# Kernel tuning notes

Hardware: AMD Instinct MI355X
Metric: run time of the kernel (lower is better)

## Reference

```python
import jax, jax.numpy as jnp
import numpy as np

B, S, D = 4, 2048, 1024

def setup_inputs() -> dict:
    key = jax.random.key(0)
    ks = jax.random.split(key, 7)
    scale = 1.0 / np.sqrt(D)
    return {
        "x": jax.random.normal(ks[0], (B, S, D), dtype=jnp.float32),
        "Wq": jax.random.uniform(ks[1], (D, D), jnp.float32, -scale, scale),
        "bq": jax.random.uniform(ks[2], (D,), jnp.float32, -scale, scale),
        "Wk": jax.random.uniform(ks[3], (D, D), jnp.float32, -scale, scale),
        "bk": jax.random.uniform(ks[4], (D,), jnp.float32, -scale, scale),
        "Wv": jax.random.uniform(ks[5], (D, D), jnp.float32, -scale, scale),
        "bv": jax.random.uniform(ks[6], (D,), jnp.float32, -scale, scale),
    }

def reference(x, Wq, bq, Wk, bk, Wv, bv):
    # Linear layers: x @ W^T + b (torch nn.Linear convention)
    q = jnp.einsum('bsd,ed->bse', x, Wq) + bq  # [B,S,D]
    k = jnp.einsum('bsd,ed->bse', x, Wk) + bk
    v = jnp.einsum('bsd,ed->bse', x, Wv) + bv
    inv_sqrt_d = 1.0 / jnp.sqrt(jnp.asarray(k.shape[-1], k.dtype))
    scores = jnp.einsum('bqd,bkd->bqk', q, k) * inv_sqrt_d  # [B,S,S]
    attn = jax.nn.softmax(scores, axis=-1)
    return jnp.einsum('bqk,bkd->bqd', attn, v)
```

## Files before the change

kernel.cpp:

```cpp
#include <hip/hip_runtime.h>
#include <cstdint>


typedef __bf16 bf16x8_t __attribute__((ext_vector_type(8)));
typedef float  f32x4_t  __attribute__((ext_vector_type(4)));
typedef int    i32x8_t  __attribute__((ext_vector_type(8)));
typedef int    i32x4_t  __attribute__((ext_vector_type(4)));

__device__ __forceinline__ uint16_t f2bf(float f) {
    union { float f; uint32_t u; } v; v.f = f;
    return (uint16_t)((v.u + 0x7fffu + ((v.u >> 16) & 1u)) >> 16);
}

__device__ __forceinline__ uint8_t f2fp8(float f) {
    union { float f; uint32_t u; } v; v.f = f;
    const uint32_t sgn = (v.u >> 31) << 7;
    const uint32_t mag = v.u & 0x7fffffffu;
    uint32_t out;
    if (mag < 0x3c800000u) {
        out = (uint32_t)__builtin_rintf(__builtin_fabsf(f) * 512.0f);
    } else {
        uint32_t t = mag + 0x7ffffu + ((mag >> 20) & 1u);
        out = (t >> 20) - 960u;
        if (out > 0x7eu) out = 0x7eu;
    }
    return (uint8_t)(sgn | out);
}

__device__ __forceinline__ void gload_lds16(const void* g, void* lds) {
    __builtin_amdgcn_global_load_lds(
        (const __attribute__((address_space(1))) void*)g,
        (__attribute__((address_space(3))) void*)lds, 16, 0, 0);
}

template <int EPI, typename OutT>
__global__ __launch_bounds__(256, 4) void gemm_bt(
    const uint16_t* __restrict__ A, int lda, long long sAz,
    const uint16_t* __restrict__ B, int ldb, long long sBz,
    OutT* __restrict__ C, int ldc, long long sCz,
    const float* __restrict__ bias0, const float* __restrict__ bias1,
    float* __restrict__ gsum, int K, float alpha)
{
    __shared__ uint16_t ldsA[128 * 64];
    __shared__ uint16_t ldsB[128 * 64];
    __shared__ float inv_denom[128];

    const int tid  = threadIdx.x;
    const int wave = tid >> 6;
    const int lane = tid & 63;
    const int quad = lane >> 4;
    const int l15  = lane & 15;
    const int z    = blockIdx.z;

    A += (long long)z * sAz;
    B += (long long)z * sBz;
    C += (long long)z * sCz;

    const int m0 = blockIdx.x * 128;
    const int n0 = blockIdx.y * 128;

    if (EPI == 4) {
        if (tid < 128) {
            const float* gp = gsum + (long long)z * 32768 + (m0 + tid) * 16;
            float s = 0.f;
#pragma unroll
            for (int t = 0; t < 16; ++t) s += gp[t];
            inv_denom[tid] = 1.f / s;
        }
    }

    const uint16_t* gA[4];
    const uint16_t* gB[4];
    uint16_t* lA[4];
    uint16_t* lB[4];
#pragma unroll
    for (int c = 0; c < 4; ++c) {
        const int s   = (c * 4 + wave) * 64 + lane;
        const int r   = s >> 3;
        const int col = ((s & 7) ^ (r & 7)) * 8;
        gA[c] = A + (long long)(m0 + r) * lda + col;
        gB[c] = B + (long long)(n0 + r) * ldb + col;
        lA[c] = ldsA + (c * 4 + wave) * 512;
        lB[c] = ldsB + (c * 4 + wave) * 512;
    }

    const int m_off = (wave & 1) * 64;
    const int n_off = (wave >> 1) * 64;

    f32x4_t acc[4][4];
#pragma unroll
    for (int i = 0; i < 4; ++i)
#pragma unroll
        for (int j = 0; j < 4; ++j)
            acc[i][j] = f32x4_t{0.f, 0.f, 0.f, 0.f};

    for (int k0 = 0; k0 < K; k0 += 64) {
#pragma unroll
        for (int c = 0; c < 4; ++c) gload_lds16(gA[c], lA[c]);
#pragma unroll
        for (int c = 0; c < 4; ++c) gload_lds16(gB[c], lB[c]);
#pragma unroll
        for (int c = 0; c < 4; ++c) { gA[c] += 64; gB[c] += 64; }
        __syncthreads();

#pragma unroll
        for (int t = 0; t < 2; ++t) {
            const int csw = ((t * 4 + quad) ^ (l15 & 7)) * 8;
            bf16x8_t af[4], bfr[4];
#pragma unroll
            for (int i = 0; i < 4; ++i)
                af[i] = *(const bf16x8_t*)(ldsA + (m_off + i * 16 + l15) * 64 + csw);
#pragma unroll
            for (int j = 0; j < 4; ++j)
                bfr[j] = *(const bf16x8_t*)(ldsB + (n_off + j * 16 + l15) * 64 + csw);
#pragma unroll
            for (int i = 0; i < 4; ++i)
#pragma unroll
                for (int j = 0; j < 4; ++j)
                    acc[i][j] = __builtin_amdgcn_mfma_f32_16x16x32_bf16(af[i], bfr[j], acc[i][j], 0, 0, 0);
        }
        __syncthreads();
    }

    if (EPI == 1 || EPI == 2) {
        const float* bias = (z == 0) ? bias0 : bias1;
#pragma unroll
        for (int i = 0; i < 4; ++i) {
            const int mb = m0 + m_off + i * 16 + quad * 4;
            float rb[4];
            if (EPI == 2) {
#pragma unroll
                for (int r = 0; r < 4; ++r) rb[r] = bias[mb + r];
            }
#pragma unroll
            for (int j = 0; j < 4; ++j) {
                const int n = n0 + n_off + j * 16 + l15;
                const float cb = (EPI == 1) ? bias[n] : 0.f;
#pragma unroll
                for (int r = 0; r < 4; ++r) {
                    const float v = acc[i][j][r] + ((EPI == 1) ? cb : rb[r]);
                    if (sizeof(OutT) == 1)
                        ((uint8_t*)C)[(long long)(mb + r) * ldc + n] = f2fp8(v);
                    else
                        ((uint16_t*)C)[(long long)(mb + r) * ldc + n] = f2bf(v);
                }
            }
        }
    } else {
#pragma unroll
        for (int i = 0; i < 4; ++i) {
            const int rl = m_off + i * 16 + quad * 4;
            const int mb = m0 + rl;
#pragma unroll
            for (int j = 0; j < 4; ++j) {
                const int n = n0 + n_off + j * 16 + l15;
#pragma unroll
                for (int r = 0; r < 4; ++r)
                    ((float*)C)[(long long)(mb + r) * ldc + n] =
                        acc[i][j][r] * inv_denom[rl + r];
            }
        }
    }
}

__global__ __launch_bounds__(256, 3) void score_f8(
    const uint8_t* __restrict__ Qf8, const uint8_t* __restrict__ Kf8,
    uint16_t* __restrict__ P, float* __restrict__ gsum, float alpha)
{
    __shared__ uint8_t ldsA[128 * 128];
    __shared__ uint8_t ldsB[128 * 128];

    const int tid  = threadIdx.x;
    const int wave = tid >> 6;
    const int lane = tid & 63;
    const int quad = lane >> 4;
    const int l15  = lane & 15;
    const int z    = blockIdx.z;

    const uint8_t* A = Qf8 + (long long)z * 2097152;
    const uint8_t* B = Kf8 + (long long)z * 2097152;
    uint16_t* C = P + (long long)z * 4194304;

    const int m0 = blockIdx.x * 128;
    const int n0 = blockIdx.y * 128;

    const uint8_t* gA[4];
    const uint8_t* gB[4];
    uint8_t* lA[4];
    uint8_t* lB[4];
#pragma unroll
    for (int c = 0; c < 4; ++c) {
        const int s   = (c * 4 + wave) * 64 + lane;
        const int r   = s >> 3;
        const int col = ((s & 7) ^ (r & 7)) * 16;
        gA[c] = A + (long long)(m0 + r) * 1024 + col;
        gB[c] = B + (long long)(n0 + r) * 1024 + col;
        lA[c] = ldsA + (c * 4 + wave) * 1024;
        lB[c] = ldsB + (c * 4 + wave) * 1024;
    }

    const int m_off = (wave & 1) * 64;
    const int n_off = (wave >> 1) * 64;

    f32x4_t acc[4][4];
#pragma unroll
    for (int i = 0; i < 4; ++i)
#pragma unroll
        for (int j = 0; j < 4; ++j)
            acc[i][j] = f32x4_t{0.f, 0.f, 0.f, 0.f};

    const int h0 = quad * 2;
    const int h1 = quad * 2 + 1;

    for (int k0 = 0; k0 < 1024; k0 += 128) {
#pragma unroll
        for (int c = 0; c < 4; ++c) gload_lds16(gA[c], lA[c]);
#pragma unroll
        for (int c = 0; c < 4; ++c) gload_lds16(gB[c], lB[c]);
#pragma unroll
        for (int c = 0; c < 4; ++c) { gA[c] += 128; gB[c] += 128; }
        __syncthreads();

        i32x8_t af[4], bfr[4];
#pragma unroll
        for (int i = 0; i < 4; ++i) {
            const int m = m_off + i * 16 + l15;
            const int sw = m & 7;
            const i32x4_t lo = *(const i32x4_t*)(ldsA + m * 128 + (h0 ^ sw) * 16);
            const i32x4_t hi = *(const i32x4_t*)(ldsA + m * 128 + (h1 ^ sw) * 16);
            af[i] = i32x8_t{lo[0], lo[1], lo[2], lo[3], hi[0], hi[1], hi[2], hi[3]};
        }
#pragma unroll
        for (int j = 0; j < 4; ++j) {
            const int n = n_off + j * 16 + l15;
            const int sw = n & 7;
            const i32x4_t lo = *(const i32x4_t*)(ldsB + n * 128 + (h0 ^ sw) * 16);
            const i32x4_t hi = *(const i32x4_t*)(ldsB + n * 128 + (h1 ^ sw) * 16);
            bfr[j] = i32x8_t{lo[0], lo[1], lo[2], lo[3], hi[0], hi[1], hi[2], hi[3]};
        }
#pragma unroll
        for (int i = 0; i < 4; ++i)
#pragma unroll
            for (int j = 0; j < 4; ++j)
                acc[i][j] = __builtin_amdgcn_mfma_scale_f32_16x16x128_f8f6f4(
                    af[i], bfr[j], acc[i][j],
                    0, 0,
                    0, 0x7f7f7f7f,
                    0, 0x7f7f7f7f);
        __syncthreads();
    }

    float rs[4][4];
#pragma unroll
    for (int i = 0; i < 4; ++i)
#pragma unroll
        for (int r = 0; r < 4; ++r) rs[i][r] = 0.f;
#pragma unroll
    for (int i = 0; i < 4; ++i) {
        const int mb = m0 + m_off + i * 16 + quad * 4;
#pragma unroll
        for (int j = 0; j < 4; ++j) {
            const int n = n0 + n_off + j * 16 + l15;
#pragma unroll
            for (int r = 0; r < 4; ++r) {
                const float e = exp2f(acc[i][j][r] * alpha);
                rs[i][r] += e;
                C[(long long)(mb + r) * 2048 + n] = f2bf(e);
            }
        }
    }
#pragma unroll
    for (int m = 1; m < 16; m <<= 1)
#pragma unroll
        for (int i = 0; i < 4; ++i)
#pragma unroll
            for (int r = 0; r < 4; ++r)
                rs[i][r] += __shfl_xor(rs[i][r], m);
    float* lp = (float*)ldsA;
    if (l15 == 0) {
#pragma unroll
        for (int i = 0; i < 4; ++i)
#pragma unroll
            for (int r = 0; r < 4; ++r)
                lp[wave * 64 + i * 16 + quad * 4 + r] = rs[i][r];
    }
    __syncthreads();
    if (tid < 128) {
        const float s = lp[(tid >> 6) * 64 + (tid & 63)] +
                        lp[((tid >> 6) + 2) * 64 + (tid & 63)];
        gsum[(long long)z * 32768 + (m0 + tid) * 16 + blockIdx.y] = s;
    }
}

__global__ void cvt_all(const float* __restrict__ x,
                        const float* __restrict__ Wq, const float* __restrict__ Wk,
                        const float* __restrict__ Wv,
                        uint16_t* __restrict__ x_bf, uint16_t* __restrict__ w_bf) {
    const int b = blockIdx.x;
    const float* src;
    uint16_t* dst;
    int i;
    if (b < 8192) {
        src = x; dst = x_bf; i = b * 256 + threadIdx.x;
    } else {
        const int wz = (b - 8192) >> 10;
        const int rb = (b - 8192) & 1023;
        src = (wz == 0) ? Wq : (wz == 1) ? Wk : Wv;
        dst = w_bf + (long long)wz * 1048576;
        i = rb * 256 + threadIdx.x;
    }
    const float4 f = ((const float4*)src)[i];
    ushort4 o;
    o.x = f2bf(f.x); o.y = f2bf(f.y); o.z = f2bf(f.z); o.w = f2bf(f.w);
    ((ushort4*)dst)[i] = o;
}

extern "C" void kernel_launch(void* const* d_in, const int* in_sizes, int n_in,
                              void* d_out, int out_size, void* d_ws, size_t ws_size,
                              hipStream_t stream) {
    const float* x  = (const float*)d_in[0];
    const float* Wq = (const float*)d_in[1];
    const float* bq = (const float*)d_in[2];
    const float* Wk = (const float*)d_in[3];
    const float* bk = (const float*)d_in[4];
    const float* Wv = (const float*)d_in[5];
    const float* bv = (const float*)d_in[6];
    float* out = (float*)d_out;

    char* w = (char*)d_ws;
    uint16_t* x_bf = (uint16_t*)(w);
    float*    gsum = (float*)(w);
    uint16_t* w_bf = (uint16_t*)(w + 16777216);
    uint8_t*  Qf8  = (uint8_t*)(w + 23068672);
    uint8_t*  Kf8  = (uint8_t*)(w + 31457280);
    uint16_t* Vt   = (uint16_t*)(w + 39845888);
    uint16_t* Pb   = (uint16_t*)(w + 56623104);

    cvt_all<<<11264, 256, 0, stream>>>(x, Wq, Wk, Wv, x_bf, w_bf);

    gemm_bt<1, uint8_t><<<dim3(64, 8, 2), 256, 0, stream>>>(
        x_bf, 1024, 0LL,
        w_bf, 1024, 1048576LL,
        Qf8, 1024, 8388608LL,
        bq, bk, nullptr, 1024, 1.0f);

    gemm_bt<2, uint16_t><<<dim3(8, 64, 1), 256, 0, stream>>>(
        w_bf + 2097152, 1024, 0LL,
        x_bf, 1024, 0LL,
        Vt, 8192, 0LL,
        bv, bv, nullptr, 1024, 1.0f);

    score_f8<<<dim3(16, 16, 4), 256, 0, stream>>>(
        Qf8, Kf8, Pb, gsum, 0.045084222f);

    gemm_bt<4, float><<<dim3(16, 8, 4), 256, 0, stream>>>(
        Pb, 2048, 4194304LL,
        Vt, 8192, 2048LL,
        out, 1024, 2097152LL,
        nullptr, nullptr, gsum, 2048, 1.0f);
}
```

Before: 235.6 us.

## Replace bf16 GEMM with 512-thread double-buffered pipelined kernel using 256-row tiles

The 128x128 single-buffered GEMM used for the Q/K, V and PV products is replaced by an 8-wave kernel with 256xBN tiles. LDS is double-buffered and global-to-LDS loads for upcoming k-tiles are interleaved with MFMA phases using explicit barriers, waitcnts and setprio. The aim is to hide load latency behind compute and raise data reuse per block. In exchange it uses more LDS and registers, has fewer blocks per launch (grid occupancy risk on the smaller GEMMs), and relies on hand-tuned vmcnt counts that are fragile.

New measurement: 260.6 us. 10.6% more time.

```diff
diff --git a/kernel.cpp b/kernel.cpp
--- a/kernel.cpp
+++ b/kernel.cpp
@@ -33,34 +33,44 @@
         (__attribute__((address_space(3))) void*)lds, 16, 0, 0);
 }
 
-template <int EPI, typename OutT>
-__global__ __launch_bounds__(256, 4) void gemm_bt(
+#define BAR()   asm volatile("s_barrier" ::: "memory")
+#define WLGKM() asm volatile("s_waitcnt lgkmcnt(0)" ::: "memory")
+
+template <int BN, int EPI, typename OutT>
+__global__ __launch_bounds__(512, 2) void gemm8p(
     const uint16_t* __restrict__ A, int lda, long long sAz,
     const uint16_t* __restrict__ B, int ldb, long long sBz,
     OutT* __restrict__ C, int ldc, long long sCz,
     const float* __restrict__ bias0, const float* __restrict__ bias1,
-    float* __restrict__ gsum, int K, float alpha)
+    const float* __restrict__ gsum, int K)
 {
-    __shared__ uint16_t ldsA[128 * 64];
-    __shared__ uint16_t ldsB[128 * 64];
-    __shared__ float inv_denom[128];
+    constexpr int NF    = BN / 64;
+    constexpr int LB    = BN / 128;
+    constexpr int BSLOT = BN * 128;
+    constexpr int BKH   = BN * 64;
+
+    __shared__ uint16_t ldsA[32768];
+    __shared__ uint16_t ldsB[BN * 128];
+    __shared__ float    inv_denom[256];
 
     const int tid  = threadIdx.x;
-    const int wave = tid >> 6;
+    const int wv   = tid >> 6;
     const int lane = tid & 63;
     const int quad = lane >> 4;
     const int l15  = lane & 15;
+    const int wm   = wv >> 2;
+    const int wn   = wv & 3;
     const int z    = blockIdx.z;
 
     A += (long long)z * sAz;
     B += (long long)z * sBz;
     C += (long long)z * sCz;
 
-    const int m0 = blockIdx.x * 128;
-    const int n0 = blockIdx.y * 128;
+    const int m0 = blockIdx.x * 256;
+    const int n0 = blockIdx.y * BN;
 
     if (EPI == 4) {
-        if (tid < 128) {
+        if (tid < 256) {
             const float* gp = gsum + (long long)z * 32768 + (m0 + tid) * 16;
             float s = 0.f;
 #pragma unroll
@@ -69,95 +79,158 @@
         }
     }
 
-    const uint16_t* gA[4];
-    const uint16_t* gB[4];
-    uint16_t* lA[4];
-    uint16_t* lB[4];
-#pragma unroll
-    for (int c = 0; c < 4; ++c) {
-        const int s   = (c * 4 + wave) * 64 + lane;
-        const int r   = s >> 3;
-        const int col = ((s & 7) ^ (r & 7)) * 8;
-        gA[c] = A + (long long)(m0 + r) * lda + col;
-        gB[c] = B + (long long)(n0 + r) * ldb + col;
-        lA[c] = ldsA + (c * 4 + wave) * 512;
-        lB[c] = ldsB + (c * 4 + wave) * 512;
-    }
-
-    const int m_off = (wave & 1) * 64;
-    const int n_off = (wave >> 1) * 64;
-
-    f32x4_t acc[4][4];
-#pragma unroll
-    for (int i = 0; i < 4; ++i)
-#pragma unroll
-        for (int j = 0; j < 4; ++j)
-            acc[i][j] = f32x4_t{0.f, 0.f, 0.f, 0.f};
-
-    for (int k0 = 0; k0 < K; k0 += 64) {
-#pragma unroll
-        for (int c = 0; c < 4; ++c) gload_lds16(gA[c], lA[c]);
-#pragma unroll
-        for (int c = 0; c < 4; ++c) gload_lds16(gB[c], lB[c]);
-#pragma unroll
-        for (int c = 0; c < 4; ++c) { gA[c] += 64; gB[c] += 64; }
-        __syncthreads();
-
-#pragma unroll
-        for (int t = 0; t < 2; ++t) {
-            const int csw = ((t * 4 + quad) ^ (l15 & 7)) * 8;
-            bf16x8_t af[4], bfr[4];
-#pragma unroll
-            for (int i = 0; i < 4; ++i)
-                af[i] = *(const bf16x8_t*)(ldsA + (m_off + i * 16 + l15) * 64 + csw);
-#pragma unroll
-            for (int j = 0; j < 4; ++j)
-                bfr[j] = *(const bf16x8_t*)(ldsB + (n_off + j * 16 + l15) * 64 + csw);
-#pragma unroll
-            for (int i = 0; i < 4; ++i)
-#pragma unroll
-                for (int j = 0; j < 4; ++j)
-                    acc[i][j] = __builtin_amdgcn_mfma_f32_16x16x32_bf16(af[i], bfr[j], acc[i][j], 0, 0, 0);
-        }
-        __syncthreads();
+    const int r  = tid >> 2;
+    const int ca = (tid & 3) ^ ((tid >> 4) & 3);
+    const uint16_t* aS = A + (long long)(m0 + r) * lda + ca * 8;
+    const uint16_t* bS = B + (long long)(n0 + r) * ldb + ca * 8;
+    const int dOf = wv * 1024;
+
+    auto STAGE_A = [&](int kt, int h, int sl) {
+        const uint16_t* s = aS + kt * 64 + h * 32;
+        char* d = (char*)ldsA + sl * 32768 + h * 16384 + dOf;
+        gload_lds16(s, d);
+        gload_lds16(s + (long long)128 * lda, d + 8192);
+    };
+    auto STAGE_B = [&](int kt, int h, int sl) {
+        const uint16_t* s = bS + kt * 64 + h * 32;
+        char* d = (char*)ldsB + sl * BSLOT + h * BKH + dOf;
+        gload_lds16(s, d);
+        if (LB == 2) gload_lds16(s + (long long)128 * ldb, d + 8192);
+    };
+
+    const int csw  = ((quad ^ (l15 >> 2)) & 3) * 16;
+    const int aOff = (wm * 128 + l15) * 64 + csw;
+    const int bOff = (wn * (BN / 4) + l15) * 64 + csw;
+
+    f32x4_t acc[8][NF];
+#pragma unroll
+    for (int i = 0; i < 8; ++i)
+#pragma unroll
+        for (int j = 0; j < NF; ++j) acc[i][j] = f32x4_t{0.f, 0.f, 0.f, 0.f};
+
+    const int NT = K >> 6;
+
+    STAGE_B(0, 0, 0); STAGE_A(0, 0, 0); STAGE_B(0, 1, 0); STAGE_A(0, 1, 0);
+    STAGE_B(1, 0, 1); STAGE_A(1, 0, 1); STAGE_B(1, 1, 1);
+    if constexpr (LB == 2) asm volatile("s_waitcnt vmcnt(6)" ::: "memory");
+    else                   asm volatile("s_waitcnt vmcnt(4)" ::: "memory");
+    BAR();
+
+    for (int t = 0; t < NT; ++t) {
+        const int sl = t & 1;
+        const int so = sl ^ 1;
+        const int t1 = (t + 1 < NT) ? t + 1 : 0;
+        const int t2 = (t + 2 < NT) ? t + 2 : 0;
+        const char* Ab = (const char*)ldsA + sl * 32768;
+        const char* Bb = (const char*)ldsB + sl * BSLOT;
+
+        bf16x8_t af[4], bfv[NF];
+
+#pragma unroll
+        for (int i = 0; i < 4; ++i)
+            af[i] = *(const bf16x8_t*)(Ab + i * 1024 + aOff);
+#pragma unroll
+        for (int j = 0; j < NF; ++j)
+            bfv[j] = *(const bf16x8_t*)(Bb + j * 1024 + bOff);
+        STAGE_A(t1, 1, so);
+        BAR(); WLGKM();
+        __builtin_amdgcn_s_setprio(1);
+#pragma unroll
+        for (int i = 0; i < 4; ++i)
+#pragma unroll
+            for (int j = 0; j < NF; ++j)
+                acc[i][j] = __builtin_amdgcn_mfma_f32_16x16x32_bf16(
+                    af[i], bfv[j], acc[i][j], 0, 0, 0);
+        __builtin_amdgcn_s_setprio(0);
+        BAR();
+
+#pragma unroll
+        for (int i = 0; i < 4; ++i)
+            af[i] = *(const bf16x8_t*)(Ab + 4096 + i * 1024 + aOff);
+        STAGE_B(t2, 0, sl);
+        BAR(); WLGKM();
+        __builtin_amdgcn_s_setprio(1);
+#pragma unroll
+        for (int i = 0; i < 4; ++i)
+#pragma unroll
+            for (int j = 0; j < NF; ++j)
+                acc[4 + i][j] = __builtin_amdgcn_mfma_f32_16x16x32_bf16(
+                    af[i], bfv[j], acc[4 + i][j], 0, 0, 0);
+        __builtin_amdgcn_s_setprio(0);
+        BAR();
+
+#pragma unroll
+        for (int i = 0; i < 4; ++i)
+            af[i] = *(const bf16x8_t*)(Ab + 16384 + i * 1024 + aOff);
+#pragma unroll
+        for (int j = 0; j < NF; ++j)
+            bfv[j] = *(const bf16x8_t*)(Bb + BKH + j * 1024 + bOff);
+        STAGE_A(t2, 0, sl);
+        BAR(); WLGKM();
+        __builtin_amdgcn_s_setprio(1);
+#pragma unroll
+        for (int i = 0; i < 4; ++i)
+#pragma unroll
+            for (int j = 0; j < NF; ++j)
+                acc[i][j] = __builtin_amdgcn_mfma_f32_16x16x32_bf16(
+                    af[i], bfv[j], acc[i][j], 0, 0, 0);
+        __builtin_amdgcn_s_setprio(0);
+        BAR();
+
+#pragma unroll
+        for (int i = 0; i < 4; ++i)
+            af[i] = *(const bf16x8_t*)(Ab + 16384 + 4096 + i * 1024 + aOff);
+        STAGE_B(t2, 1, sl);
+        BAR(); WLGKM();
+        __builtin_amdgcn_s_setprio(1);
+#pragma unroll
+        for (int i = 0; i < 4; ++i)
+#pragma unroll
+            for (int j = 0; j < NF; ++j)
+                acc[4 + i][j] = __builtin_amdgcn_mfma_f32_16x16x32_bf16(
+                    af[i], bfv[j], acc[4 + i][j], 0, 0, 0);
+        __builtin_amdgcn_s_setprio(0);
+        if constexpr (LB == 2) asm volatile("s_waitcnt vmcnt(6)" ::: "memory");
+        else                   asm volatile("s_waitcnt vmcnt(4)" ::: "memory");
+        BAR();
     }
 
     if (EPI == 1 || EPI == 2) {
         const float* bias = (z == 0) ? bias0 : bias1;
 #pragma unroll
-        for (int i = 0; i < 4; ++i) {
-            const int mb = m0 + m_off + i * 16 + quad * 4;
+        for (int fi = 0; fi < 8; ++fi) {
+            const int mb = m0 + wm * 128 + fi * 16 + quad * 4;
             float rb[4];
             if (EPI == 2) {
 #pragma unroll
-                for (int r = 0; r < 4; ++r) rb[r] = bias[mb + r];
+                for (int rr = 0; rr < 4; ++rr) rb[rr] = bias[mb + rr];
             }
 #pragma unroll
-            for (int j = 0; j < 4; ++j) {
-                const int n = n0 + n_off + j * 16 + l15;
+            for (int fj = 0; fj < NF; ++fj) {
+                const int n = n0 + wn * (BN / 4) + fj * 16 + l15;
                 const float cb = (EPI == 1) ? bias[n] : 0.f;
 #pragma unroll
-                for (int r = 0; r < 4; ++r) {
-                    const float v = acc[i][j][r] + ((EPI == 1) ? cb : rb[r]);
+                for (int rr = 0; rr < 4; ++rr) {
+                    const float vv = acc[fi][fj][rr] + ((EPI == 1) ? cb : rb[rr]);
                     if (sizeof(OutT) == 1)
-                        ((uint8_t*)C)[(long long)(mb + r) * ldc + n] = f2fp8(v);
+                        ((uint8_t*)C)[(long long)(mb + rr) * ldc + n] = f2fp8(vv);
                     else
-                        ((uint16_t*)C)[(long long)(mb + r) * ldc + n] = f2bf(v);
+                        ((uint16_t*)C)[(long long)(mb + rr) * ldc + n] = f2bf(vv);
                 }
             }
         }
     } else {
 #pragma unroll
-        for (int i = 0; i < 4; ++i) {
-            const int rl = m_off + i * 16 + quad * 4;
+        for (int fi = 0; fi < 8; ++fi) {
+            const int rl = wm * 128 + fi * 16 + quad * 4;
             const int mb = m0 + rl;
 #pragma unroll
-            for (int j = 0; j < 4; ++j) {
-                const int n = n0 + n_off + j * 16 + l15;
-#pragma unroll
-                for (int r = 0; r < 4; ++r)
-                    ((float*)C)[(long long)(mb + r) * ldc + n] =
-                        acc[i][j][r] * inv_denom[rl + r];
+            for (int fj = 0; fj < NF; ++fj) {
+                const int n = n0 + wn * (BN / 4) + fj * 16 + l15;
+#pragma unroll
+                for (int rr = 0; rr < 4; ++rr)
+                    ((float*)C)[(long long)(mb + rr) * ldc + n] =
+                        acc[fi][fj][rr] * inv_denom[rl + rr];
             }
         }
     }
@@ -338,24 +411,24 @@
 
     cvt_all<<<11264, 256, 0, stream>>>(x, Wq, Wk, Wv, x_bf, w_bf);
 
-    gemm_bt<1, uint8_t><<<dim3(64, 8, 2), 256, 0, stream>>>(
+    gemm8p<256, 1, uint8_t><<<dim3(32, 4, 2), 512, 0, stream>>>(
         x_bf, 1024, 0LL,
         w_bf, 1024, 1048576LL,
         Qf8, 1024, 8388608LL,
-        bq, bk, nullptr, 1024, 1.0f);
-
-    gemm_bt<2, uint16_t><<<dim3(8, 64, 1), 256, 0, stream>>>(
+        bq, bk, nullptr, 1024);
+
+    gemm8p<128, 2, uint16_t><<<dim3(4, 64, 1), 512, 0, stream>>>(
         w_bf + 2097152, 1024, 0LL,
         x_bf, 1024, 0LL,
         Vt, 8192, 0LL,
-        bv, bv, nullptr, 1024, 1.0f);
+        bv, bv, nullptr, 1024);
 
     score_f8<<<dim3(16, 16, 4), 256, 0, stream>>>(
         Qf8, Kf8, Pb, gsum, 0.045084222f);
 
-    gemm_bt<4, float><<<dim3(16, 8, 4), 256, 0, stream>>>(
+    gemm8p<128, 4, float><<<dim3(8, 8, 4), 512, 0, stream>>>(
         Pb, 2048, 4194304LL,
         Vt, 8192, 2048LL,
         out, 1024, 2097152LL,
-        nullptr, nullptr, gsum, 2048, 1.0f);
-}
+        nullptr, nullptr, gsum, 2048);
+}
```
